# Performance work log

Measured on AMD Instinct MI355X. Metric: run time of the kernel, lower is better.

The kernel has to match this reference:

```python
import jax
import jax.numpy as jnp
import numpy as np

IN_FEATS = 784
HIDDEN_DIM = 1024
BATCH = 1024


def setup_inputs() -> dict:
    key = jax.random.key(0)
    k_px, k_W, k_c, k_V, k_b = jax.random.split(key, 5)
    pixels = jax.random.uniform(k_px, (BATCH, IN_FEATS), dtype=jnp.float32)
    W = jax.random.normal(k_W, (HIDDEN_DIM, IN_FEATS), dtype=jnp.float32)
    c = jax.random.normal(k_c, (HIDDEN_DIM,), dtype=jnp.float32)
    V = jax.random.normal(k_V, (IN_FEATS, HIDDEN_DIM), dtype=jnp.float32)
    b = jax.random.normal(k_b, (IN_FEATS,), dtype=jnp.float32)
    return {"pixels": pixels, "W": W, "c": c, "V": V, "b": b}


def reference(pixels, W, c, V, b):
    # pixels: [B, D]; W: [H, D]; c: [H]; V: [D, H]; b: [D]
    B = pixels.shape[0]
    a0 = jnp.broadcast_to(c[None, :], (B, c.shape[0]))  # [B, H]

    def step(a, inp):
        w_col, v_row, b_i, x_i = inp  # [H], [H], [], [B]
        h = jax.nn.sigmoid(a)                     # [B, H]
        pred_i = b_i + h @ v_row                  # [B]
        a_next = a + w_col[None, :] * x_i[:, None]  # rank-1 accumulator update
        return a_next, pred_i

    xs = (W.T, V, b, pixels.T)  # each leading dim D (scan over visible units)
    _, preds = jax.lax.scan(step, a0, xs)  # preds: [D, B]
    return preds.T  # [B, D]
```

## Files before the change

kernel.cpp:

```cpp
#include <hip/hip_runtime.h>
#include <stdint.h>

#define B_ 1024
#define D_ 784
#define H_ 1024
#define BH_ (B_ * H_)
#define LOG2E 1.4426950408889634f


typedef float v2f __attribute__((ext_vector_type(2)));

__device__ __forceinline__ unsigned short bf16_rne(float x) {
    unsigned b = __float_as_uint(x);
    return (unsigned short)((b + 0x7FFFu + ((b >> 16) & 1u)) >> 16);
}

__device__ __forceinline__ int seg_bound(int s) {
    const int b[5] = {0, 200, 392, 592, 784};
    return b[s];
}

__global__ __launch_bounds__(256) void prep(const float* __restrict__ V,
                                            const float* __restrict__ W,
                                            const float* __restrict__ px,
                                            unsigned short* __restrict__ VWb,
                                            float* __restrict__ G) {
    __shared__ float smem[1056];
    const int t = threadIdx.x;

    if (blockIdx.x < 800) {
        int i0 = (blockIdx.x % 25) * 32;
        int h0 = (blockIdx.x / 25) * 32;
        int tx = t & 31, ty = t >> 5;
        int hb = h0 >> 8, hr = h0 & 255;
#pragma unroll
        for (int j = 0; j < 4; ++j) {
            int i = i0 + ty + j * 8;
            if (i < D_)
                VWb[((size_t)i * 4 + hb) * 512 + hr + tx] = bf16_rne(V[(size_t)i * H_ + h0 + tx]);
        }
#pragma unroll
        for (int j = 0; j < 4; ++j) {
            int h = h0 + ty + j * 8;
            int i = i0 + tx;
            float v = 0.f;
            if (i < D_) v = W[(size_t)h * D_ + i] * LOG2E;
            smem[(ty + j * 8) * 33 + tx] = v;
        }
        __syncthreads();
#pragma unroll
        for (int j = 0; j < 4; ++j) {
            int i = i0 + ty + j * 8;
            if (i < D_)
                VWb[((size_t)i * 4 + hb) * 512 + 256 + hr + tx] = bf16_rne(smem[tx * 33 + ty + j * 8]);
        }
    } else {
        float* xs = smem;
        float* ws = smem + 512;
        int idx = blockIdx.x - 800;
        int r   = idx >> 8;
        int b0  = (idx & 15) * 64;
        int h0  = ((idx >> 4) & 15) * 64;
        int j0s = seg_bound(r), j1s = seg_bound(r + 1);

        const int tb = t >> 4, th = t & 15;
        float acc[4][4];
#pragma unroll
        for (int bi = 0; bi < 4; ++bi)
#pragma unroll
            for (int hh = 0; hh < 4; ++hh) acc[bi][hh] = 0.f;

        const int xb = t >> 3;
        const int xj = t & 7;
        const int wh = t >> 1, wj = (t & 1) * 4;

        for (int j0 = j0s; j0 < j1s; j0 += 8) {
            float xv0 = px[(size_t)(b0 + xb) * D_ + j0 + xj];
            float xv1 = px[(size_t)(b0 + 32 + xb) * D_ + j0 + xj];
            float4 wv = make_float4(0, 0, 0, 0);
            if (t < 128) wv = *(const float4*)(W + (size_t)(h0 + wh) * D_ + j0 + wj);
            __syncthreads();
            xs[xj * 64 + xb]      = xv0;
            xs[xj * 64 + 32 + xb] = xv1;
            if (t < 128) {
                ws[(wj + 0) * 64 + wh] = wv.x * LOG2E;
                ws[(wj + 1) * 64 + wh] = wv.y * LOG2E;
                ws[(wj + 2) * 64 + wh] = wv.z * LOG2E;
                ws[(wj + 3) * 64 + wh] = wv.w * LOG2E;
            }
            __syncthreads();
#pragma unroll
            for (int jj = 0; jj < 8; ++jj) {
                float4 xq = *(float4*)&xs[jj * 64 + tb * 4];
                float4 wq = *(float4*)&ws[jj * 64 + th * 4];
                float xa[4] = {xq.x, xq.y, xq.z, xq.w};
                float wa[4] = {wq.x, wq.y, wq.z, wq.w};
#pragma unroll
                for (int bi = 0; bi < 4; ++bi)
#pragma unroll
                    for (int hh = 0; hh < 4; ++hh)
                        acc[bi][hh] = fmaf(xa[bi], wa[hh], acc[bi][hh]);
            }
        }
        float* dst = G + (size_t)r * BH_;
#pragma unroll
        for (int bi = 0; bi < 4; ++bi) {
            float4 o = make_float4(acc[bi][0], acc[bi][1], acc[bi][2], acc[bi][3]);
            *(float4*)(dst + (size_t)(b0 + tb * 4 + bi) * H_ + h0 + th * 4) = o;
        }
    }
}

template <int CTRL>
__device__ __forceinline__ float dpp_add(float p) {
    int s = __builtin_amdgcn_update_dpp(0, __float_as_int(p), CTRL, 0xf, 0xf, true);
    return p + __int_as_float(s);
}
__device__ __forceinline__ float reduce64(float p) {
    p = dpp_add<0x111>(p);
    p = dpp_add<0x112>(p);
    p = dpp_add<0x114>(p);
    p = dpp_add<0x118>(p);
    p = dpp_add<0x142>(p);
    p = dpp_add<0x143>(p);
    return p;
}

__device__ __forceinline__ void unpack_pair(const uint4& uA, const uint4& uB, v2f (&o)[8]) {
    o[0].x = __uint_as_float(uA.x << 16); o[0].y = __uint_as_float(uB.x << 16);
    o[1].x = __uint_as_float(uA.x);       o[1].y = __uint_as_float(uB.x);
    o[2].x = __uint_as_float(uA.y << 16); o[2].y = __uint_as_float(uB.y << 16);
    o[3].x = __uint_as_float(uA.y);       o[3].y = __uint_as_float(uB.y);
    o[4].x = __uint_as_float(uA.z << 16); o[4].y = __uint_as_float(uB.z << 16);
    o[5].x = __uint_as_float(uA.z);       o[5].y = __uint_as_float(uB.z);
    o[6].x = __uint_as_float(uA.w << 16); o[6].y = __uint_as_float(uB.w << 16);
    o[7].x = __uint_as_float(uA.w);       o[7].y = __uint_as_float(uB.w);
}

__device__ __forceinline__ void tree16(v2f (&Aq)[8],
                                       const uint4& uvA, const uint4& uwA,
                                       const uint4& uvB, const uint4& uwB,
                                       float xi, v2f& n, v2f& d) {
    v2f va[8], wa[8];
    unpack_pair(uvA, uvB, va);
    unpack_pair(uwA, uwB, wa);
    const v2f one = {1.f, 1.f};
    v2f xiv; xiv.x = xi; xiv.y = xi;
    v2f q[8];
#pragma unroll
    for (int k = 0; k < 8; ++k) {
        float ex = __builtin_amdgcn_exp2f(fminf(15.f, -Aq[k].x));
        float ey = __builtin_amdgcn_exp2f(fminf(15.f, -Aq[k].y));
        v2f e; e.x = ex; e.y = ey;
        q[k] = one + e;
        Aq[k] = wa[k] * xiv + Aq[k];
    }
    v2f a01 = va[0] * q[1] + va[1] * q[0];
    v2f a23 = va[2] * q[3] + va[3] * q[2];
    v2f a45 = va[4] * q[5] + va[5] * q[4];
    v2f a67 = va[6] * q[7] + va[7] * q[6];
    v2f q01 = q[0] * q[1], q23 = q[2] * q[3];
    v2f q45 = q[4] * q[5], q67 = q[6] * q[7];
    v2f n0123 = a01 * q23 + a23 * q01;
    v2f n4567 = a45 * q67 + a67 * q45;
    v2f q0123 = q01 * q23, q4567 = q45 * q67;
    d = q0123 * q4567;
    n = n0123 * q4567 + n4567 * q0123;
}

__global__ __launch_bounds__(256, 4) void nade_main(
    const float* __restrict__ px,
    const float* __restrict__ c,
    const unsigned short* __restrict__ VWb,
    const float* __restrict__ G,
    const float* __restrict__ bias,
    float* __restrict__ out)
{
    const int lane = threadIdx.x & 63;
    const int wid  = threadIdx.x >> 6;
    const int bid  = blockIdx.x;
    const int s    = bid >> 8;
    const int rb   = bid & 255;
    const int row  = rb * 4 + wid;

    const int i0s = seg_bound(s), i1s = seg_bound(s + 1);

    const int hA = lane * 8;
    const int hB = 512 + hA;

    v2f Aq[8];
    {
        float4 c0 = *(const float4*)(c + hA);
        float4 c1 = *(const float4*)(c + hA + 4);
        float4 c2 = *(const float4*)(c + hB);
        float4 c3 = *(const float4*)(c + hB + 4);
        Aq[0].x = c0.x * LOG2E; Aq[0].y = c2.x * LOG2E;
        Aq[1].x = c0.y * LOG2E; Aq[1].y = c2.y * LOG2E;
        Aq[2].x = c0.z * LOG2E; Aq[2].y = c2.z * LOG2E;
        Aq[3].x = c0.w * LOG2E; Aq[3].y = c2.w * LOG2E;
        Aq[4].x = c1.x * LOG2E; Aq[4].y = c3.x * LOG2E;
        Aq[5].x = c1.y * LOG2E; Aq[5].y = c3.y * LOG2E;
        Aq[6].x = c1.z * LOG2E; Aq[6].y = c3.z * LOG2E;
        Aq[7].x = c1.w * LOG2E; Aq[7].y = c3.w * LOG2E;
        for (int r = 0; r < s; ++r) {
            const float* gp = G + (size_t)r * BH_ + (size_t)row * H_;
            float4 g0 = *(const float4*)(gp + hA);
            float4 g1 = *(const float4*)(gp + hA + 4);
            float4 g2 = *(const float4*)(gp + hB);
            float4 g3 = *(const float4*)(gp + hB + 4);
            Aq[0].x += g0.x; Aq[0].y += g2.x;
            Aq[1].x += g0.y; Aq[1].y += g2.y;
            Aq[2].x += g0.z; Aq[2].y += g2.z;
            Aq[3].x += g0.w; Aq[3].y += g2.w;
            Aq[4].x += g1.x; Aq[4].y += g3.x;
            Aq[5].x += g1.y; Aq[5].y += g3.y;
            Aq[6].x += g1.z; Aq[6].y += g3.z;
            Aq[7].x += g1.w; Aq[7].y += g3.w;
        }
    }

    const float* xp = px + (size_t)row * D_;
    const uint4* vw = (const uint4*)VWb + (size_t)i0s * 256 + (lane >> 5) * 64 + (lane & 31);

    uint4 vA = vw[0], wA = vw[32], vB = vw[128], wB = vw[160];
    vw += 256;
    float4 xq = *(const float4*)(xp + i0s);

    for (int ib = i0s; ib < i1s; ib += 4) {
        int xb = (ib + 4 < i1s) ? (ib + 4) : i0s;
        float4 xq_n = *(const float4*)(xp + xb);
        float xa[4] = {xq.x, xq.y, xq.z, xq.w};
        float pr[4];
#pragma unroll
        for (int j = 0; j < 4; ++j) {
            uint4 vAn = vw[0], wAn = vw[32], vBn = vw[128], wBn = vw[160];
            vw += 256;
            v2f n, d;
            tree16(Aq, vA, wA, vB, wB, xa[j], n, d);
            float p = fmaf(n.x, __builtin_amdgcn_rcpf(d.x),
                           n.y * __builtin_amdgcn_rcpf(d.y));
            pr[j] = reduce64(p);
            vA = vAn; wA = wAn; vB = vBn; wB = wBn;
        }
        float4 b4 = *(const float4*)(bias + ib);
        if (lane == 63) {
            float4 o = make_float4(pr[0] + b4.x, pr[1] + b4.y, pr[2] + b4.z, pr[3] + b4.w);
            *(float4*)(out + (size_t)row * D_ + ib) = o;
        }
        xq = xq_n;
    }
}

extern "C" void kernel_launch(void* const* d_in, const int* in_sizes, int n_in,
                              void* d_out, int out_size, void* d_ws, size_t ws_size,
                              hipStream_t stream) {
    const float* px   = (const float*)d_in[0];
    const float* W    = (const float*)d_in[1];
    const float* c    = (const float*)d_in[2];
    const float* V    = (const float*)d_in[3];
    const float* bias = (const float*)d_in[4];
    float* out = (float*)d_out;

    unsigned short* VWb = (unsigned short*)d_ws;
    float* G    = (float*)((char*)d_ws + (size_t)788 * 4096);

    prep<<<dim3(1568), 256, 0, stream>>>(V, W, px, VWb, G);

    nade_main<<<dim3(1024), 256, 0, stream>>>(px, c, VWb, G, bias, out);
}
```

Measured before the change: 318.4 us.

## Store V/W in fp32 interleaved layout, negate accumulator, reorder block-to-segment mapping

Replaces the bf16 packed V/W buffer with an fp32 buffer laid out so each lane's pair-interleaved elements load directly as v2f. This removes the per-step unpack shifts and the in-loop negation by storing -LOG2E*W and keeping a negated accumulator. It also interleaves the segment index into the low block-id bits so blocks from different segments run concurrently, and drops the software prefetch of the next step's operands. The cost is twice the bytes per step read from the workspace and more global-load pressure without explicit double buffering.

```diff
diff --git a/kernel.cpp b/kernel.cpp
--- a/kernel.cpp
+++ b/kernel.cpp
@@ -10,20 +10,19 @@
 
 typedef float v2f __attribute__((ext_vector_type(2)));
 
-__device__ __forceinline__ unsigned short bf16_rne(float x) {
-    unsigned b = __float_as_uint(x);
-    return (unsigned short)((b + 0x7FFFu + ((b >> 16) & 1u)) >> 16);
-}
-
 __device__ __forceinline__ int seg_bound(int s) {
     const int b[5] = {0, 200, 392, 592, 784};
     return b[s];
 }
 
+__device__ __forceinline__ size_t vw_idx(int i, int h, int part) {
+    return (size_t)i * 2048 + part * 1024 + ((h & 511) >> 3) * 16 + (h & 7) * 2 + (h >> 9);
+}
+
 __global__ __launch_bounds__(256) void prep(const float* __restrict__ V,
                                             const float* __restrict__ W,
                                             const float* __restrict__ px,
-                                            unsigned short* __restrict__ VWb,
+                                            float* __restrict__ VWf,
                                             float* __restrict__ G) {
     __shared__ float smem[1056];
     const int t = threadIdx.x;
@@ -32,19 +31,18 @@
         int i0 = (blockIdx.x % 25) * 32;
         int h0 = (blockIdx.x / 25) * 32;
         int tx = t & 31, ty = t >> 5;
-        int hb = h0 >> 8, hr = h0 & 255;
 #pragma unroll
         for (int j = 0; j < 4; ++j) {
             int i = i0 + ty + j * 8;
             if (i < D_)
-                VWb[((size_t)i * 4 + hb) * 512 + hr + tx] = bf16_rne(V[(size_t)i * H_ + h0 + tx]);
+                VWf[vw_idx(i, h0 + tx, 0)] = V[(size_t)i * H_ + h0 + tx];
         }
 #pragma unroll
         for (int j = 0; j < 4; ++j) {
             int h = h0 + ty + j * 8;
             int i = i0 + tx;
             float v = 0.f;
-            if (i < D_) v = W[(size_t)h * D_ + i] * LOG2E;
+            if (i < D_) v = W[(size_t)h * D_ + i] * -LOG2E;
             smem[(ty + j * 8) * 33 + tx] = v;
         }
         __syncthreads();
@@ -52,7 +50,7 @@
         for (int j = 0; j < 4; ++j) {
             int i = i0 + ty + j * 8;
             if (i < D_)
-                VWb[((size_t)i * 4 + hb) * 512 + 256 + hr + tx] = bf16_rne(smem[tx * 33 + ty + j * 8]);
+                VWf[vw_idx(i, h0 + tx, 1)] = smem[tx * 33 + ty + j * 8];
         }
     } else {
         float* xs = smem;
@@ -126,34 +124,20 @@
     return p;
 }
 
-__device__ __forceinline__ void unpack_pair(const uint4& uA, const uint4& uB, v2f (&o)[8]) {
-    o[0].x = __uint_as_float(uA.x << 16); o[0].y = __uint_as_float(uB.x << 16);
-    o[1].x = __uint_as_float(uA.x);       o[1].y = __uint_as_float(uB.x);
-    o[2].x = __uint_as_float(uA.y << 16); o[2].y = __uint_as_float(uB.y << 16);
-    o[3].x = __uint_as_float(uA.y);       o[3].y = __uint_as_float(uB.y);
-    o[4].x = __uint_as_float(uA.z << 16); o[4].y = __uint_as_float(uB.z << 16);
-    o[5].x = __uint_as_float(uA.z);       o[5].y = __uint_as_float(uB.z);
-    o[6].x = __uint_as_float(uA.w << 16); o[6].y = __uint_as_float(uB.w << 16);
-    o[7].x = __uint_as_float(uA.w);       o[7].y = __uint_as_float(uB.w);
-}
-
-__device__ __forceinline__ void tree16(v2f (&Aq)[8],
-                                       const uint4& uvA, const uint4& uwA,
-                                       const uint4& uvB, const uint4& uwB,
+__device__ __forceinline__ void tree16(v2f (&An)[8], const float4 (&Va)[4], const float4 (&Wa)[4],
                                        float xi, v2f& n, v2f& d) {
-    v2f va[8], wa[8];
-    unpack_pair(uvA, uvB, va);
-    unpack_pair(uwA, uwB, wa);
+    const v2f* va = (const v2f*)&Va[0];
+    const v2f* wa = (const v2f*)&Wa[0];
     const v2f one = {1.f, 1.f};
     v2f xiv; xiv.x = xi; xiv.y = xi;
     v2f q[8];
 #pragma unroll
     for (int k = 0; k < 8; ++k) {
-        float ex = __builtin_amdgcn_exp2f(fminf(15.f, -Aq[k].x));
-        float ey = __builtin_amdgcn_exp2f(fminf(15.f, -Aq[k].y));
-        v2f e; e.x = ex; e.y = ey;
+        v2f e;
+        e.x = __builtin_amdgcn_exp2f(fminf(15.f, An[k].x));
+        e.y = __builtin_amdgcn_exp2f(fminf(15.f, An[k].y));
         q[k] = one + e;
-        Aq[k] = wa[k] * xiv + Aq[k];
+        An[k] = wa[k] * xiv + An[k];
     }
     v2f a01 = va[0] * q[1] + va[1] * q[0];
     v2f a23 = va[2] * q[3] + va[3] * q[2];
@@ -171,7 +155,7 @@
 __global__ __launch_bounds__(256, 4) void nade_main(
     const float* __restrict__ px,
     const float* __restrict__ c,
-    const unsigned short* __restrict__ VWb,
+    const float* __restrict__ VWf,
     const float* __restrict__ G,
     const float* __restrict__ bias,
     float* __restrict__ out)
@@ -179,8 +163,8 @@
     const int lane = threadIdx.x & 63;
     const int wid  = threadIdx.x >> 6;
     const int bid  = blockIdx.x;
-    const int s    = bid >> 8;
-    const int rb   = bid & 255;
+    const int s    = (bid >> 1) & 3;
+    const int rb   = ((bid >> 3) << 1) | (bid & 1);
     const int row  = rb * 4 + wid;
 
     const int i0s = seg_bound(s), i1s = seg_bound(s + 1);
@@ -188,42 +172,40 @@
     const int hA = lane * 8;
     const int hB = 512 + hA;
 
-    v2f Aq[8];
+    v2f An[8];
     {
         float4 c0 = *(const float4*)(c + hA);
         float4 c1 = *(const float4*)(c + hA + 4);
         float4 c2 = *(const float4*)(c + hB);
         float4 c3 = *(const float4*)(c + hB + 4);
-        Aq[0].x = c0.x * LOG2E; Aq[0].y = c2.x * LOG2E;
-        Aq[1].x = c0.y * LOG2E; Aq[1].y = c2.y * LOG2E;
-        Aq[2].x = c0.z * LOG2E; Aq[2].y = c2.z * LOG2E;
-        Aq[3].x = c0.w * LOG2E; Aq[3].y = c2.w * LOG2E;
-        Aq[4].x = c1.x * LOG2E; Aq[4].y = c3.x * LOG2E;
-        Aq[5].x = c1.y * LOG2E; Aq[5].y = c3.y * LOG2E;
-        Aq[6].x = c1.z * LOG2E; Aq[6].y = c3.z * LOG2E;
-        Aq[7].x = c1.w * LOG2E; Aq[7].y = c3.w * LOG2E;
+        An[0].x = -c0.x * LOG2E; An[0].y = -c2.x * LOG2E;
+        An[1].x = -c0.y * LOG2E; An[1].y = -c2.y * LOG2E;
+        An[2].x = -c0.z * LOG2E; An[2].y = -c2.z * LOG2E;
+        An[3].x = -c0.w * LOG2E; An[3].y = -c2.w * LOG2E;
+        An[4].x = -c1.x * LOG2E; An[4].y = -c3.x * LOG2E;
+        An[5].x = -c1.y * LOG2E; An[5].y = -c3.y * LOG2E;
+        An[6].x = -c1.z * LOG2E; An[6].y = -c3.z * LOG2E;
+        An[7].x = -c1.w * LOG2E; An[7].y = -c3.w * LOG2E;
         for (int r = 0; r < s; ++r) {
             const float* gp = G + (size_t)r * BH_ + (size_t)row * H_;
             float4 g0 = *(const float4*)(gp + hA);
             float4 g1 = *(const float4*)(gp + hA + 4);
             float4 g2 = *(const float4*)(gp + hB);
             float4 g3 = *(const float4*)(gp + hB + 4);
-            Aq[0].x += g0.x; Aq[0].y += g2.x;
-            Aq[1].x += g0.y; Aq[1].y += g2.y;
-            Aq[2].x += g0.z; Aq[2].y += g2.z;
-            Aq[3].x += g0.w; Aq[3].y += g2.w;
-            Aq[4].x += g1.x; Aq[4].y += g3.x;
-            Aq[5].x += g1.y; Aq[5].y += g3.y;
-            Aq[6].x += g1.z; Aq[6].y += g3.z;
-            Aq[7].x += g1.w; Aq[7].y += g3.w;
+            An[0].x -= g0.x; An[0].y -= g2.x;
+            An[1].x -= g0.y; An[1].y -= g2.y;
+            An[2].x -= g0.z; An[2].y -= g2.z;
+            An[3].x -= g0.w; An[3].y -= g2.w;
+            An[4].x -= g1.x; An[4].y -= g3.x;
+            An[5].x -= g1.y; An[5].y -= g3.y;
+            An[6].x -= g1.z; An[6].y -= g3.z;
+            An[7].x -= g1.w; An[7].y -= g3.w;
         }
     }
 
     const float* xp = px + (size_t)row * D_;
-    const uint4* vw = (const uint4*)VWb + (size_t)i0s * 256 + (lane >> 5) * 64 + (lane & 31);
-
-    uint4 vA = vw[0], wA = vw[32], vB = vw[128], wB = vw[160];
-    vw += 256;
+    const float4* vp = (const float4*)VWf + (size_t)i0s * 512 + lane * 4;
+
     float4 xq = *(const float4*)(xp + i0s);
 
     for (int ib = i0s; ib < i1s; ib += 4) {
@@ -233,14 +215,15 @@
         float pr[4];
 #pragma unroll
         for (int j = 0; j < 4; ++j) {
-            uint4 vAn = vw[0], wAn = vw[32], vBn = vw[128], wBn = vw[160];
-            vw += 256;
+            float4 Va[4], Wa[4];
+#pragma unroll
+            for (int u = 0; u < 4; ++u) { Va[u] = vp[u]; Wa[u] = vp[256 + u]; }
+            vp += 512;
             v2f n, d;
-            tree16(Aq, vA, wA, vB, wB, xa[j], n, d);
+            tree16(An, Va, Wa, xa[j], n, d);
             float p = fmaf(n.x, __builtin_amdgcn_rcpf(d.x),
                            n.y * __builtin_amdgcn_rcpf(d.y));
             pr[j] = reduce64(p);
-            vA = vAn; wA = wAn; vB = vBn; wB = wBn;
         }
         float4 b4 = *(const float4*)(bias + ib);
         if (lane == 63) {
@@ -261,10 +244,10 @@
     const float* bias = (const float*)d_in[4];
     float* out = (float*)d_out;
 
-    unsigned short* VWb = (unsigned short*)d_ws;
-    float* G    = (float*)((char*)d_ws + (size_t)788 * 4096);
-
-    prep<<<dim3(1568), 256, 0, stream>>>(V, W, px, VWb, G);
-
-    nade_main<<<dim3(1024), 256, 0, stream>>>(px, c, VWb, G, bias, out);
-}
+    float* VWf = (float*)d_ws;
+    float* G   = (float*)((char*)d_ws + (size_t)788 * 8192);
+
+    prep<<<dim3(1568), 256, 0, stream>>>(V, W, px, VWf, G);
+
+    nade_main<<<dim3(1024), 256, 0, stream>>>(px, c, VWf, G, bias, out);
+}
```

Measured after the change: 471.2 us. 48.0% more time.
